# Optimization experiments

Hardware: AMD Instinct MI355X
Metric: run time of the kernel (lower is better)

The kernel has to match this reference:

```python
import jax, jax.numpy as jnp
import numpy as np

LN_EPS = 1e-5


def setup_inputs() -> dict:
    key = jax.random.key(0)
    ks = jax.random.split(key, 12)
    b, m, d = 4096, 64, 256
    s = 1.0 / np.sqrt(d)
    return {
        "head_left": jax.random.normal(ks[0], (b, d), jnp.float32),
        "rel_left": jax.random.normal(ks[1], (b, m, d), jnp.float32),
        "tail_left": jax.random.normal(ks[2], (b, m, d), jnp.float32),
        "head_right": jax.random.normal(ks[3], (b, d), jnp.float32),
        "rel_right": jax.random.normal(ks[4], (b, m, d), jnp.float32),
        "tail_right": jax.random.normal(ks[5], (b, m, d), jnp.float32),
        "mask_left": jax.random.randint(ks[6], (b, m), 0, 2).astype(bool),
        "mask_right": jax.random.randint(ks[7], (b, m), 0, 2).astype(bool),
        "bilinear_w": jax.random.normal(ks[8], (d, d), jnp.float32) * s,
        "w_tail": jax.random.normal(ks[9], (d, d), jnp.float32) * s,
        "w_head": jax.random.normal(ks[10], (d, d), jnp.float32) * s,
        "ln_gamma": jnp.ones((d,), jnp.float32),
        "ln_beta": jnp.zeros((d,), jnp.float32),
    }


def _intra_attention(weak_rel, rel, tail, mask, bilinear_w):
    # score[b,m] = weak_rel[b,:] @ W @ rel[b,m,:]  (nn.Bilinear with out=1, no bias)
    hW = weak_rel @ bilinear_w                      # [b, d]
    score = jnp.einsum("bd,bmd->bm", hW, rel)       # [b, m]
    score = jnp.where(mask, -jnp.inf, score)
    att = jax.nn.softmax(score, axis=1)             # [b, m]
    return jnp.einsum("bm,bmd->bd", att, tail)      # weighted sum of tails


def _layer_norm(x, gamma, beta):
    mu = jnp.mean(x, axis=-1, keepdims=True)
    var = jnp.var(x, axis=-1, keepdims=True)
    return (x - mu) * jax.lax.rsqrt(var + LN_EPS) * gamma + beta


def reference(head_left, rel_left, tail_left, head_right, rel_right, tail_right,
              mask_left, mask_right, bilinear_w, w_tail, w_head, ln_gamma, ln_beta):
    weak_rel = head_right - head_left
    left = _intra_attention(weak_rel, rel_left, tail_left, mask_left, bilinear_w)
    right = _intra_attention(weak_rel, rel_right, tail_right, mask_right, bilinear_w)
    # torch Linear: x @ W.T ; dropout p=0.0 is identity
    left = jax.nn.relu(left @ w_tail.T + head_left @ w_head.T)
    right = jax.nn.relu(right @ w_tail.T + head_right @ w_head.T)
    left = _layer_norm(left + head_left, ln_gamma, ln_beta)
    right = _layer_norm(right + head_right, ln_gamma, ln_beta)
    return (left, right)
```

## Files before the change

### kernel.cpp

```cpp
#include <hip/hip_runtime.h>

#define NB 4096
#define MM 64
#define DD 256
#define LN_EPS 1e-5f
#define NEG_BIG -1e30f

typedef float f4v __attribute__((ext_vector_type(4)));

#define WS_WCAT 0
#define WS_HW   (512 * DD)
#define WS_CTX  (WS_HW + NB * DD)

__global__ __launch_bounds__(256)
void k_prep(const float* __restrict__ head_left,
            const float* __restrict__ head_right,
            const float* __restrict__ bw,
            const float* __restrict__ wt,
            const float* __restrict__ wh,
            float* __restrict__ wcat,
            float* __restrict__ hW)
{
    __shared__ float smem[64 * 65];
    const int t = threadIdx.x;

    if (blockIdx.x < 32) {
        const int mat   = blockIdx.x >> 4;
        const int tile  = blockIdx.x & 15;
        const int dBase = (tile >> 2) * 64;
        const int kBase = (tile & 3) * 64;
        const float* __restrict__ w = mat ? wh : wt;
        float (*tile_s)[65] = (float(*)[65])smem;
        const int c  = t & 63;
        const int rr = t >> 6;
        #pragma unroll
        for (int r = rr; r < 64; r += 4)
            tile_s[r][c] = w[(dBase + r) * DD + kBase + c];
        __syncthreads();
        #pragma unroll
        for (int kr = rr; kr < 64; kr += 4)
            wcat[(mat * 256 + kBase + kr) * DD + dBase + c] = tile_s[c][kr];
    } else {
        const int blk  = blockIdx.x - 32;
        const int lane = t & 63;
        const int w    = t >> 6;
        float (*weak_s)[DD] = (float(*)[DD])smem;
        #pragma unroll
        for (int r = 0; r < 16; ++r) {
            const size_t idx = (size_t)(blk * 16 + r) * DD + t;
            weak_s[r][t] = head_right[idx] - head_left[idx];
        }
        __syncthreads();

        float4 acc[4];
        #pragma unroll
        for (int r = 0; r < 4; ++r) acc[r] = make_float4(0.f, 0.f, 0.f, 0.f);
        for (int k = 0; k < DD; ++k) {
            const float4 w4 = *(const float4*)(bw + k * DD + 4 * lane);
            #pragma unroll
            for (int r = 0; r < 4; ++r) {
                const float x = weak_s[4 * w + r][k];
                acc[r].x += x * w4.x; acc[r].y += x * w4.y;
                acc[r].z += x * w4.z; acc[r].w += x * w4.w;
            }
        }
        #pragma unroll
        for (int r = 0; r < 4; ++r)
            *(float4*)(hW + (size_t)(blk * 16 + 4 * w + r) * DD + 4 * lane) = acc[r];
    }
}

__global__ __launch_bounds__(256)
void k_attn(const float* __restrict__ rel_left,
            const float* __restrict__ tail_left,
            const float* __restrict__ rel_right,
            const float* __restrict__ tail_right,
            const unsigned char* __restrict__ mask_left,
            const unsigned char* __restrict__ mask_right,
            const float* __restrict__ hW,
            float* __restrict__ ctx)
{
    const int b    = blockIdx.x >> 1;
    const int side = blockIdx.x & 1;
    const int t    = threadIdx.x;
    const int lane = t & 63;
    const int w    = t >> 6;

    const float* __restrict__ rel  = side ? rel_right  : rel_left;
    const float* __restrict__ tail = side ? tail_right : tail_left;
    const unsigned char* __restrict__ mask = side ? mask_right : mask_left;

    __shared__ float part_s[MM][65];
    __shared__ float red_s[MM][5];
    __shared__ float att_s[MM];
    __shared__ float cpart_s[4][DD];

    const float4 hw4 = *(const float4*)(hW + (size_t)b * DD + 4 * lane);
    const float* rp = rel  + (size_t)b * MM * DD + 4 * lane;
    const float* tp = tail + (size_t)b * MM * DD + 4 * lane;

    #pragma unroll
    for (int i = 0; i < 16; ++i) {
        const int m = w * 16 + i;
        const f4v r4 = __builtin_nontemporal_load((const f4v*)(rp + (size_t)m * DD));
        part_s[m][lane] = hw4.x * r4.x + hw4.y * r4.y + hw4.z * r4.z + hw4.w * r4.w;
    }
    __syncthreads();

    {
        const int m = t & 63;
        const int c = t >> 6;
        float s = 0.f;
        #pragma unroll
        for (int j = 0; j < 16; ++j) s += part_s[m][c * 16 + j];
        red_s[m][c] = s;
    }
    __syncthreads();

    if (w == 0) {
        const unsigned char v0 = mask_left[lane];
        const bool mask_u8 = (__ballot(((lane & 3) != 0) && (v0 != 0)) != 0ULL);

        float s = red_s[lane][0] + red_s[lane][1] + red_s[lane][2] + red_s[lane][3];
        const bool msk = mask_u8
            ? (mask[(size_t)b * MM + lane] != 0)
            : (((const int*)(const void*)mask)[(size_t)b * MM + lane] != 0);
        if (msk) s = NEG_BIG;
        float mx = s;
        #pragma unroll
        for (int off = 32; off >= 1; off >>= 1) mx = fmaxf(mx, __shfl_xor(mx, off, 64));
        const float e = __expf(s - mx);
        float sum = e;
        #pragma unroll
        for (int off = 32; off >= 1; off >>= 1) sum += __shfl_xor(sum, off, 64);
        att_s[lane] = e / sum;
    }
    __syncthreads();

    float4 acc = make_float4(0.f, 0.f, 0.f, 0.f);
    #pragma unroll 4
    for (int i = 0; i < 16; ++i) {
        const int m = w * 16 + i;
        const float a  = att_s[m];
        const f4v v = __builtin_nontemporal_load((const f4v*)(tp + (size_t)m * DD));
        acc.x += a * v.x; acc.y += a * v.y; acc.z += a * v.z; acc.w += a * v.w;
    }
    *(float4*)(&cpart_s[w][4 * lane]) = acc;
    __syncthreads();

    const float sum = cpart_s[0][t] + cpart_s[1][t] + cpart_s[2][t] + cpart_s[3][t];
    ctx[(size_t)(side * NB + b) * DD + t] = sum;
}

__global__ __launch_bounds__(256)
void k_outln(const float* __restrict__ ctx,
             const float* __restrict__ head_left,
             const float* __restrict__ head_right,
             const float* __restrict__ wcat,
             const float* __restrict__ gamma,
             const float* __restrict__ beta,
             float* __restrict__ out)
{
    const int blk  = blockIdx.x;
    const int t    = threadIdx.x;
    const int lane = t & 63;
    const int w    = t >> 6;

    const int rg0  = __builtin_amdgcn_readfirstlane(blk * 32 + w * 8);
    const int side = rg0 >> 12;
    const int bb0  = rg0 & (NB - 1);
    const float* __restrict__ head = side ? head_right : head_left;

    float4 acc[8];
    #pragma unroll
    for (int r = 0; r < 8; ++r) acc[r] = make_float4(0.f, 0.f, 0.f, 0.f);

    {
        const float* __restrict__ xr = ctx + (size_t)rg0 * DD;
        #pragma unroll 4
        for (int k = 0; k < 256; ++k) {
            const float4 w4 = *(const float4*)(wcat + (size_t)k * DD + 4 * lane);
            #pragma unroll
            for (int r = 0; r < 8; ++r) {
                const float x = xr[r * DD + k];
                acc[r].x += x * w4.x; acc[r].y += x * w4.y;
                acc[r].z += x * w4.z; acc[r].w += x * w4.w;
            }
        }
    }
    {
        const float* __restrict__ xh = head + (size_t)bb0 * DD;
        #pragma unroll 4
        for (int k = 0; k < 256; ++k) {
            const float4 w4 = *(const float4*)(wcat + (size_t)(256 + k) * DD + 4 * lane);
            #pragma unroll
            for (int r = 0; r < 8; ++r) {
                const float x = xh[r * DD + k];
                acc[r].x += x * w4.x; acc[r].y += x * w4.y;
                acc[r].z += x * w4.z; acc[r].w += x * w4.w;
            }
        }
    }

    const float4 g4 = *(const float4*)(gamma + 4 * lane);
    const float4 b4 = *(const float4*)(beta  + 4 * lane);

    #pragma unroll
    for (int r = 0; r < 8; ++r) {
        const int rg = rg0 + r;
        const int bb = rg & (NB - 1);
        const float4 h4 = *(const float4*)(head + (size_t)bb * DD + 4 * lane);
        float4 y;
        y.x = fmaxf(acc[r].x, 0.f) + h4.x;
        y.y = fmaxf(acc[r].y, 0.f) + h4.y;
        y.z = fmaxf(acc[r].z, 0.f) + h4.z;
        y.w = fmaxf(acc[r].w, 0.f) + h4.w;

        float s1 = y.x + y.y + y.z + y.w;
        float s2 = y.x * y.x + y.y * y.y + y.z * y.z + y.w * y.w;
        #pragma unroll
        for (int off = 32; off >= 1; off >>= 1) {
            s1 += __shfl_xor(s1, off, 64);
            s2 += __shfl_xor(s2, off, 64);
        }
        const float mu   = s1 * (1.0f / DD);
        const float var  = s2 * (1.0f / DD) - mu * mu;
        const float rstd = rsqrtf(var + LN_EPS);

        f4v o;
        o.x = (y.x - mu) * rstd * g4.x + b4.x;
        o.y = (y.y - mu) * rstd * g4.y + b4.y;
        o.z = (y.z - mu) * rstd * g4.z + b4.z;
        o.w = (y.w - mu) * rstd * g4.w + b4.w;
        __builtin_nontemporal_store(o, (f4v*)(out + (size_t)rg * DD + 4 * lane));
    }
}

extern "C" void kernel_launch(void* const* d_in, const int* in_sizes, int n_in,
                              void* d_out, int out_size, void* d_ws, size_t ws_size,
                              hipStream_t stream) {
    const float* head_left  = (const float*)d_in[0];
    const float* rel_left   = (const float*)d_in[1];
    const float* tail_left  = (const float*)d_in[2];
    const float* head_right = (const float*)d_in[3];
    const float* rel_right  = (const float*)d_in[4];
    const float* tail_right = (const float*)d_in[5];
    const unsigned char* mask_left  = (const unsigned char*)d_in[6];
    const unsigned char* mask_right = (const unsigned char*)d_in[7];
    const float* bw    = (const float*)d_in[8];
    const float* wt    = (const float*)d_in[9];
    const float* wh    = (const float*)d_in[10];
    const float* gamma = (const float*)d_in[11];
    const float* beta  = (const float*)d_in[12];
    float* out = (float*)d_out;

    float* ws   = (float*)d_ws;
    float* wcat = ws + WS_WCAT;
    float* hW   = ws + WS_HW;
    float* ctxb = ws + WS_CTX;

    k_prep <<<dim3(288),  dim3(256), 0, stream>>>(head_left, head_right, bw, wt, wh, wcat, hW);
    k_attn <<<dim3(8192), dim3(256), 0, stream>>>(rel_left, tail_left, rel_right, tail_right,
                                                  mask_left, mask_right, hW, ctxb);
    k_outln<<<dim3(256),  dim3(256), 0, stream>>>(ctxb, head_left, head_right, wcat,
                                                  gamma, beta, out);
}
```

Baseline: 254.1 us.

## Replace scalar FP32 output GEMM with bf16 MFMA and packed operands

The output projection GEMM (context and head times the concatenated tail/head weights) moves from scalar FP32 FMAs to bf16 MFMA 16x16x32 instructions. The attention kernel now writes its context directly as bf16 into a concatenated A matrix. The prep kernel converts the head rows and a pre-packed B layout to bf16 so the fused kernel can feed MFMA directly. The intent is to cut the compute cost of the final GEMM, at the price of bf16 rounding of activations and weights before layer norm.

```diff
diff --git a/kernel.cpp b/kernel.cpp
--- a/kernel.cpp
+++ b/kernel.cpp
@@ -1,4 +1,5 @@
 #include <hip/hip_runtime.h>
+#include <hip/hip_bf16.h>
 
 #define NB 4096
 #define MM 64
@@ -7,10 +8,15 @@
 #define NEG_BIG -1e30f
 
 typedef float f4v __attribute__((ext_vector_type(4)));
-
-#define WS_WCAT 0
-#define WS_HW   (512 * DD)
-#define WS_CTX  (WS_HW + NB * DD)
+typedef __attribute__((ext_vector_type(8))) short bf16x8;
+typedef __attribute__((ext_vector_type(4))) float f32x4;
+
+#define WS_HW 0
+
+__device__ inline unsigned short f2bf(float x) {
+    __hip_bfloat16 h = __float2bfloat16(x);
+    return *reinterpret_cast<unsigned short*>(&h);
+}
 
 __global__ __launch_bounds__(256)
 void k_prep(const float* __restrict__ head_left,
@@ -18,30 +24,40 @@
             const float* __restrict__ bw,
             const float* __restrict__ wt,
             const float* __restrict__ wh,
-            float* __restrict__ wcat,
+            short* __restrict__ A_bf,
+            short* __restrict__ Bp,
             float* __restrict__ hW)
 {
-    __shared__ float smem[64 * 65];
+    __shared__ float smem[16 * DD];
     const int t = threadIdx.x;
 
-    if (blockIdx.x < 32) {
-        const int mat   = blockIdx.x >> 4;
-        const int tile  = blockIdx.x & 15;
-        const int dBase = (tile >> 2) * 64;
-        const int kBase = (tile & 3) * 64;
-        const float* __restrict__ w = mat ? wh : wt;
-        float (*tile_s)[65] = (float(*)[65])smem;
-        const int c  = t & 63;
-        const int rr = t >> 6;
-        #pragma unroll
-        for (int r = rr; r < 64; r += 4)
-            tile_s[r][c] = w[(dBase + r) * DD + kBase + c];
-        __syncthreads();
-        #pragma unroll
-        for (int kr = rr; kr < 64; kr += 4)
-            wcat[(mat * 256 + kBase + kr) * DD + dBase + c] = tile_s[c][kr];
+    if (blockIdx.x < 16) {
+        const int kb = blockIdx.x;
+        const float* __restrict__ src = (kb < 8) ? wt : wh;
+        const int kbase = (kb & 7) * 32;
+        const int c = t;
+        unsigned int words[16];
+        #pragma unroll
+        for (int i = 0; i < 16; ++i) {
+            const float a = src[c * DD + kbase + 2 * i];
+            const float b = src[c * DD + kbase + 2 * i + 1];
+            words[i] = (unsigned int)f2bf(a) | ((unsigned int)f2bf(b) << 16);
+        }
+        uint4* dst = (uint4*)(Bp + ((size_t)kb * 256 + c) * 32);
+        #pragma unroll
+        for (int i = 0; i < 4; ++i) dst[i] = *(uint4*)&words[4 * i];
+    } else if (blockIdx.x < 48) {
+        const int hb   = blockIdx.x - 16;
+        const int rg0  = hb * 256;
+        const int side = rg0 >> 12;
+        const int bb0  = rg0 & (NB - 1);
+        const float* __restrict__ head = side ? head_right : head_left;
+        for (int r = 0; r < 256; ++r) {
+            const float v = head[(size_t)(bb0 + r) * DD + t];
+            A_bf[(size_t)(rg0 + r) * 512 + 256 + t] = (short)f2bf(v);
+        }
     } else {
-        const int blk  = blockIdx.x - 32;
+        const int blk  = blockIdx.x - 48;
         const int lane = t & 63;
         const int w    = t >> 6;
         float (*weak_s)[DD] = (float(*)[DD])smem;
@@ -78,7 +94,7 @@
             const unsigned char* __restrict__ mask_left,
             const unsigned char* __restrict__ mask_right,
             const float* __restrict__ hW,
-            float* __restrict__ ctx)
+            short* __restrict__ A_bf)
 {
     const int b    = blockIdx.x >> 1;
     const int side = blockIdx.x & 1;
@@ -149,72 +165,67 @@
     __syncthreads();
 
     const float sum = cpart_s[0][t] + cpart_s[1][t] + cpart_s[2][t] + cpart_s[3][t];
-    ctx[(size_t)(side * NB + b) * DD + t] = sum;
-}
-
-__global__ __launch_bounds__(256)
-void k_outln(const float* __restrict__ ctx,
-             const float* __restrict__ head_left,
-             const float* __restrict__ head_right,
-             const float* __restrict__ wcat,
-             const float* __restrict__ gamma,
-             const float* __restrict__ beta,
-             float* __restrict__ out)
+    A_bf[(size_t)(side * NB + b) * 512 + t] = (short)f2bf(sum);
+}
+
+__global__ __launch_bounds__(512)
+void k_fuse(const short* __restrict__ A_bf,
+            const short* __restrict__ Bp,
+            const float* __restrict__ head_left,
+            const float* __restrict__ head_right,
+            const float* __restrict__ gamma,
+            const float* __restrict__ beta,
+            float* __restrict__ out)
 {
     const int blk  = blockIdx.x;
     const int t    = threadIdx.x;
     const int lane = t & 63;
     const int w    = t >> 6;
-
-    const int rg0  = __builtin_amdgcn_readfirstlane(blk * 32 + w * 8);
-    const int side = rg0 >> 12;
-    const int bb0  = rg0 & (NB - 1);
+    const int wr   = w >> 2;
+    const int wc   = w & 3;
+    const int rg0  = blk * 32;
+
+    __shared__ float x_s[32][260];
+
+    f32x4 acc[4] = {f32x4{0,0,0,0}, f32x4{0,0,0,0}, f32x4{0,0,0,0}, f32x4{0,0,0,0}};
+
+    const short* ap = A_bf + (size_t)(rg0 + wr * 16 + (lane & 15)) * 512 + (lane >> 4) * 8;
+    const short* bp = Bp + (size_t)(wc * 64 + (lane & 15)) * 32 + (lane >> 4) * 8;
+
+    #pragma unroll 4
+    for (int ks = 0; ks < 16; ++ks) {
+        const bf16x8 a = *(const bf16x8*)(ap + ks * 32);
+        #pragma unroll
+        for (int ct = 0; ct < 4; ++ct) {
+            const bf16x8 b = *(const bf16x8*)(bp + (size_t)ks * 8192 + ct * 512);
+            acc[ct] = __builtin_amdgcn_mfma_f32_16x16x32_bf16(a, b, acc[ct], 0, 0, 0);
+        }
+    }
+
+    #pragma unroll
+    for (int ct = 0; ct < 4; ++ct)
+        #pragma unroll
+        for (int q = 0; q < 4; ++q)
+            x_s[wr * 16 + (lane >> 4) * 4 + q][wc * 64 + ct * 16 + (lane & 15)] = acc[ct][q];
+    __syncthreads();
+
+    const int  side = rg0 >> 12;
     const float* __restrict__ head = side ? head_right : head_left;
-
-    float4 acc[8];
-    #pragma unroll
-    for (int r = 0; r < 8; ++r) acc[r] = make_float4(0.f, 0.f, 0.f, 0.f);
-
-    {
-        const float* __restrict__ xr = ctx + (size_t)rg0 * DD;
-        #pragma unroll 4
-        for (int k = 0; k < 256; ++k) {
-            const float4 w4 = *(const float4*)(wcat + (size_t)k * DD + 4 * lane);
-            #pragma unroll
-            for (int r = 0; r < 8; ++r) {
-                const float x = xr[r * DD + k];
-                acc[r].x += x * w4.x; acc[r].y += x * w4.y;
-                acc[r].z += x * w4.z; acc[r].w += x * w4.w;
-            }
-        }
-    }
-    {
-        const float* __restrict__ xh = head + (size_t)bb0 * DD;
-        #pragma unroll 4
-        for (int k = 0; k < 256; ++k) {
-            const float4 w4 = *(const float4*)(wcat + (size_t)(256 + k) * DD + 4 * lane);
-            #pragma unroll
-            for (int r = 0; r < 8; ++r) {
-                const float x = xh[r * DD + k];
-                acc[r].x += x * w4.x; acc[r].y += x * w4.y;
-                acc[r].z += x * w4.z; acc[r].w += x * w4.w;
-            }
-        }
-    }
-
     const float4 g4 = *(const float4*)(gamma + 4 * lane);
     const float4 b4 = *(const float4*)(beta  + 4 * lane);
 
     #pragma unroll
-    for (int r = 0; r < 8; ++r) {
+    for (int rr = 0; rr < 4; ++rr) {
+        const int r  = 4 * w + rr;
         const int rg = rg0 + r;
         const int bb = rg & (NB - 1);
+        const float4 v  = *(const float4*)(&x_s[r][4 * lane]);
         const float4 h4 = *(const float4*)(head + (size_t)bb * DD + 4 * lane);
         float4 y;
-        y.x = fmaxf(acc[r].x, 0.f) + h4.x;
-        y.y = fmaxf(acc[r].y, 0.f) + h4.y;
-        y.z = fmaxf(acc[r].z, 0.f) + h4.z;
-        y.w = fmaxf(acc[r].w, 0.f) + h4.w;
+        y.x = fmaxf(v.x, 0.f) + h4.x;
+        y.y = fmaxf(v.y, 0.f) + h4.y;
+        y.z = fmaxf(v.z, 0.f) + h4.z;
+        y.w = fmaxf(v.w, 0.f) + h4.w;
 
         float s1 = y.x + y.y + y.z + y.w;
         float s2 = y.x * y.x + y.y * y.y + y.z * y.z + y.w * y.w;
@@ -255,13 +266,14 @@
     float* out = (float*)d_out;
 
     float* ws   = (float*)d_ws;
-    float* wcat = ws + WS_WCAT;
     float* hW   = ws + WS_HW;
-    float* ctxb = ws + WS_CTX;
-
-    k_prep <<<dim3(288),  dim3(256), 0, stream>>>(head_left, head_right, bw, wt, wh, wcat, hW);
+    short* A_bf = (short*)(ws + NB * DD);
+    short* Bp   = A_bf + (size_t)8192 * 512;
+
+    k_prep <<<dim3(304),  dim3(256), 0, stream>>>(head_left, head_right, bw, wt, wh,
+                                                  A_bf, Bp, hW);
     k_attn <<<dim3(8192), dim3(256), 0, stream>>>(rel_left, tail_left, rel_right, tail_right,
-                                                  mask_left, mask_right, hW, ctxb);
-    k_outln<<<dim3(256),  dim3(256), 0, stream>>>(ctxb, head_left, head_right, wcat,
+                                                  mask_left, mask_right, hW, A_bf);
+    k_fuse <<<dim3(256),  dim3(512), 0, stream>>>(A_bf, Bp, head_left, head_right,
                                                   gamma, beta, out);
 }
```

New measurement: 209.8 us. 17.5% less time.
